# Kernel tuning notes

Measured on AMD Instinct MI355X. Metric: run time of the kernel, lower is better.

The kernel has to match this reference:

```python
import jax, jax.numpy as jnp
import numpy as np

N, E, T, R, L = 100000, 800000, 2, 4, 2
DIN, H, C, DOUT = 16, 256, 128, 4
EPS = 1e-5


def hetero_linear(x, node_type, W, b):
    # y[i] = x[i] @ W[node_type[i]] + b[node_type[i]]; small fixed T loop
    out = jnp.zeros((x.shape[0], W.shape[-1]), x.dtype)
    for t in range(W.shape[0]):
        out = out + jnp.where((node_type == t)[:, None], x @ W[t] + b[t], jnp.zeros((), x.dtype))
    return out


def hetero_bn(x, node_type, gamma, beta):
    # per-node-type batch norm (training-mode statistics, biased variance)
    T_ = gamma.shape[0]
    cnt = jax.ops.segment_sum(jnp.ones((x.shape[0],), x.dtype), node_type, num_segments=T_)
    cnt = jnp.maximum(cnt, 1.0)[:, None]
    mean = jax.ops.segment_sum(x, node_type, num_segments=T_) / cnt
    var = jax.ops.segment_sum(x * x, node_type, num_segments=T_) / cnt - mean * mean
    inv = jax.lax.rsqrt(var + EPS)
    return (x - mean[node_type]) * inv[node_type] * gamma[node_type] + beta[node_type]


def rgcn_conv(x, edge_index, edge_type, W, root, bias):
    # RGCNConv with sum aggregation: out_i = x_i @ root + b + sum_{(j->i), r} x_j @ W_r
    src, dst = edge_index[0], edge_index[1]
    hs = jnp.einsum('nd,rdf->rnf', x, W)          # [R, N, C]
    msg = hs[edge_type, src]                       # [E, C] per-edge relation-transformed source feats
    agg = jax.ops.segment_sum(msg, dst, num_segments=x.shape[0])
    return agg + x @ root + bias


def setup_inputs() -> dict:
    key = jax.random.key(0)
    ks = iter(jax.random.split(key, 40))

    def w(shape, fan_in):
        return jax.random.normal(next(ks), shape, jnp.float32) / np.float32(np.sqrt(fan_in))

    inp = {}
    inp['x'] = jax.random.normal(next(ks), (N, DIN), jnp.float32)
    inp['edge_index'] = jax.random.randint(next(ks), (2, E), 0, N)
    inp['node_type'] = jax.random.randint(next(ks), (N,), 0, T)
    inp['edge_type'] = jax.random.randint(next(ks), (E,), 0, R)
    inp['ri_w0'] = w((T, DIN, H), DIN); inp['ri_b0'] = jnp.zeros((T, H))
    inp['ri_g0'] = jnp.ones((T, H)); inp['ri_be0'] = jnp.zeros((T, H))
    inp['ri_w1'] = w((T, H, C), H); inp['ri_b1'] = jnp.zeros((T, C))
    inp['cn_g'] = jnp.ones((L, T, C)); inp['cn_b'] = jnp.zeros((L, T, C))
    inp['rg_w'] = w((L, R, C, C), C); inp['rg_root'] = w((L, C, C), C); inp['rg_bias'] = jnp.zeros((L, C))
    inp['mn_g'] = jnp.ones((L, T, C)); inp['mn_b'] = jnp.zeros((L, T, C))
    inp['mw0'] = w((L, T, C, H), C); inp['mb0'] = jnp.zeros((L, T, H))
    inp['mg0'] = jnp.ones((L, T, H)); inp['mbe0'] = jnp.zeros((L, T, H))
    inp['mw1'] = w((L, T, H, C), H); inp['mb1'] = jnp.zeros((L, T, C))
    inp['ro_w0'] = w((T, C, H), C); inp['ro_b0'] = jnp.zeros((T, H))
    inp['ro_g0'] = jnp.ones((T, H)); inp['ro_be0'] = jnp.zeros((T, H))
    inp['ro_w1'] = w((T, H, DOUT), H); inp['ro_b1'] = jnp.zeros((T, DOUT))
    return inp


def reference(x, edge_index, node_type, edge_type,
              ri_w0, ri_b0, ri_g0, ri_be0, ri_w1, ri_b1,
              cn_g, cn_b, rg_w, rg_root, rg_bias,
              mn_g, mn_b, mw0, mb0, mg0, mbe0, mw1, mb1,
              ro_w0, ro_b0, ro_g0, ro_be0, ro_w1, ro_b1):
    act = jax.nn.leaky_relu  # negative_slope 0.01, as nn.LeakyReLU default
    # readin MLP (plain_last)
    h = hetero_linear(x, node_type, ri_w0, ri_b0)
    h = act(hetero_bn(h, node_type, ri_g0, ri_be0))
    h = hetero_linear(h, node_type, ri_w1, ri_b1)
    # RES+ blocks: Norm -> Act -> Conv -> +res, Norm -> Act -> MLP -> +res (dropout=0)
    for l in range(rg_w.shape[0]):
        y = act(hetero_bn(h, node_type, cn_g[l], cn_b[l]))
        h = h + rgcn_conv(y, edge_index, edge_type, rg_w[l], rg_root[l], rg_bias[l])
        y = act(hetero_bn(h, node_type, mn_g[l], mn_b[l]))
        y = hetero_linear(y, node_type, mw0[l], mb0[l])
        y = act(hetero_bn(y, node_type, mg0[l], mbe0[l]))
        y = hetero_linear(y, node_type, mw1[l], mb1[l])
        h = h + y
    # readout MLP (plain_last)
    h = hetero_linear(h, node_type, ro_w0, ro_b0)
    h = act(hetero_bn(h, node_type, ro_g0, ro_be0))
    return hetero_linear(h, node_type, ro_w1, ro_b1)
```

## Files before the change

### kernel.cpp

```cpp
#include <hip/hip_runtime.h>

#define TT 2
#define RR 4
#define LL 2
#define DIN 16
#define HH 256
#define CC 128
#define DOUT 4
#define EPS 1e-5f
#define NB 32
#define NBG 16

typedef float v4f __attribute__((ext_vector_type(4)));
typedef short bf16x8 __attribute__((ext_vector_type(8)));

__device__ __forceinline__ ushort f2bf(float x) {
    uint u = __float_as_uint(x);
    return (ushort)((u + 0x7fffu + ((u >> 16) & 1u)) >> 16);
}
__device__ __forceinline__ float bf2f(ushort h) { return __uint_as_float(((uint)h) << 16); }
__device__ __forceinline__ int swc(int c) { return c ^ ((c >> 3) & 7); }
__device__ __forceinline__ uint pack2(float x, float y) {
    return (uint)f2bf(x) | ((uint)f2bf(y) << 16);
}

__global__ __launch_bounds__(1024) void k_scan1(const int* __restrict__ in, int* __restrict__ out,
                                                int* __restrict__ part, int n) {
    __shared__ int sm[1024];
    const int tid = threadIdx.x;
    const int i = blockIdx.x * 1024 + tid;
    const int v = (i < n) ? in[i] : 0;
    sm[tid] = v;
    __syncthreads();
    for (int off = 1; off < 1024; off <<= 1) {
        const int u = (tid >= off) ? sm[tid - off] : 0;
        __syncthreads();
        sm[tid] += u;
        __syncthreads();
    }
    if (i < n) out[i] = sm[tid] - v;
    if (tid == 1023) part[blockIdx.x] = sm[1023];
}

__global__ __launch_bounds__(1024) void k_scan2(int* __restrict__ part, int nb) {
    __shared__ int sm[1024];
    const int tid = threadIdx.x;
    const int v = (tid < nb) ? part[tid] : 0;
    sm[tid] = v;
    __syncthreads();
    for (int off = 1; off < 1024; off <<= 1) {
        const int u = (tid >= off) ? sm[tid - off] : 0;
        __syncthreads();
        sm[tid] += u;
        __syncthreads();
    }
    if (tid < nb) part[tid] = sm[tid] - v;
    if (tid == nb - 1) part[nb] = sm[tid];
}

__global__ __launch_bounds__(1024) void k_scan3(int* __restrict__ arr, const int* __restrict__ part,
                                                int n, int nb, int* __restrict__ typeStart,
                                                int* __restrict__ out2) {
    const int i = blockIdx.x * 1024 + threadIdx.x;
    if (i < n) {
        const int v = arr[i] + part[i >> 10];
        arr[i] = v;
        if (out2) out2[i] = v;
    } else if (i == n) {
        const int total = part[nb];
        arr[n] = total;
        if (typeStart) { typeStart[0] = 0; typeStart[1] = n - total; typeStart[2] = n; }
    }
}

__global__ __launch_bounds__(256) void k_build_perm(const int* __restrict__ nt, const int* __restrict__ pscan,
                                                    const int* __restrict__ typeStart, int* __restrict__ perm,
                                                    int* __restrict__ inv, int n) {
    const int i = blockIdx.x * 256 + threadIdx.x;
    if (i >= n) return;
    const int s1 = pscan[i];
    const int pos = nt[i] ? (typeStart[1] + s1) : (i - s1);
    perm[pos] = i;
    inv[i] = pos;
}

__global__ __launch_bounds__(256) void k_deg2(const int* __restrict__ dstv, const int* __restrict__ et,
                                              const int* __restrict__ inv, int* __restrict__ rowp2, int nE) {
    const int e = blockIdx.x * 256 + threadIdx.x;
    if (e < nE) atomicAdd(&rowp2[inv[dstv[e]] * 4 + et[e]], 1);
}

__global__ __launch_bounds__(256) void k_fill2(const int* __restrict__ srcv, const int* __restrict__ dstv,
                                               const int* __restrict__ et, const int* __restrict__ inv,
                                               int* __restrict__ cur, int* __restrict__ csr, int nE) {
    const int e = blockIdx.x * 256 + threadIdx.x;
    if (e < nE) {
        const int pos = atomicAdd(&cur[inv[dstv[e]] * 4 + et[e]], 1);
        csr[pos] = inv[srcv[e]];
    }
}

__global__ __launch_bounds__(256) void k_packall(const float* __restrict__ ri_w1, const float* __restrict__ mw0,
                                                 const float* __restrict__ mw1, const float* __restrict__ ro_w0,
                                                 ushort* __restrict__ p_ri1, ushort* __restrict__ p_mw0,
                                                 ushort* __restrict__ p_mw1, ushort* __restrict__ p_ro0) {
    for (long long idx = (long long)blockIdx.x * 256 + threadIdx.x; idx < 393216;
         idx += (long long)gridDim.x * 256) {
        const float* src; ushort* dst; int K, N; long long lo;
        if (idx < 65536)       { src = ri_w1; dst = p_ri1; K = 256; N = 128; lo = idx; }
        else if (idx < 196608) { src = mw0;   dst = p_mw0; K = 128; N = 256; lo = idx - 65536; }
        else if (idx < 327680) { src = mw1;   dst = p_mw1; K = 256; N = 128; lo = idx - 196608; }
        else                   { src = ro_w0; dst = p_ro0; K = 128; N = 256; lo = idx - 327680; }
        const int kn = K * N;
        const int mat = (int)(lo / kn);
        const int rem = (int)(lo - (long long)mat * kn);
        const int k = rem / N, col = rem % N;
        dst[((size_t)mat * (K / 8) + (k >> 3)) * N * 8 + (size_t)col * 8 + (k & 7)] = f2bf(src[lo]);
    }
}

__global__ __launch_bounds__(256) void k_pack_conv(const float* __restrict__ rgw_all,
                                                   const float* __restrict__ root_all,
                                                   ushort* __restrict__ dst_all) {
    const int idx = blockIdx.x * 256 + threadIdx.x;
    if (idx >= 640 * 128) return;
    const int l = blockIdx.y;
    const float* rgw = rgw_all + (size_t)l * RR * CC * CC;
    const float* root = root_all + (size_t)l * CC * CC;
    ushort* dst = dst_all + (size_t)l * 640 * 128;
    const int k = idx >> 7, col = idx & 127;
    const float v = (k < 512) ? rgw[(((k >> 7) * CC) + (k & 127)) * CC + col]
                              : root[(size_t)(k - 512) * CC + col];
    dst[((size_t)(k >> 3) * CC + col) * 8 + (k & 7)] = f2bf(v);
}

__global__ __launch_bounds__(512) void k_coef(const float* __restrict__ stat, const int* __restrict__ typeStart,
                                              const float* __restrict__ g, const float* __restrict__ be,
                                              float* __restrict__ scale, float* __restrict__ shift, int F) {
    const int tid = threadIdx.x;
    if (tid >= TT * F) return;
    const int t = tid / F;
    float s = 0.f, q = 0.f;
    for (int b = 0; b < NB; ++b) {
        s += stat[(size_t)b * 1024 + tid];
        q += stat[(size_t)b * 1024 + 512 + tid];
    }
    const float cnt = fmaxf((float)(typeStart[t + 1] - typeStart[t]), 1.f);
    const float mean = s / cnt;
    const float var = q / cnt - mean * mean;
    const float sc = g[tid] * rsqrtf(var + EPS);
    scale[tid] = sc;
    shift[tid] = be[tid] - mean * sc;
}

__global__ __launch_bounds__(256) void k_bnact(const float* __restrict__ h, const float* __restrict__ scale,
                                               const float* __restrict__ shift, const int* __restrict__ typeStart,
                                               ushort* __restrict__ y16, int n) {
    const int c0 = typeStart[1];
    const long long total = (long long)n * 32;
    for (long long idx = (long long)blockIdx.x * 256 + threadIdx.x; idx < total;
         idx += (long long)gridDim.x * 256) {
        const int i = (int)(idx >> 5), cq = (int)(idx & 31);
        const int t = (i >= c0) ? 1 : 0;
        const v4f v = *(const v4f*)(h + (size_t)i * CC + cq * 4);
        const v4f sc = *(const v4f*)(scale + t * CC + cq * 4);
        const v4f sf = *(const v4f*)(shift + t * CC + cq * 4);
        float o[4];
#pragma unroll
        for (int j = 0; j < 4; ++j) {
            const float vv = fmaf(v[j], sc[j], sf[j]);
            o[j] = fmaxf(vv, 0.01f * vv);
        }
        uint2 p = make_uint2(pack2(o[0], o[1]), pack2(o[2], o[3]));
        *(uint2*)((uint*)y16 + (size_t)i * 64 + cq * 2) = p;
    }
}

__global__ __launch_bounds__(256) void k_agg4(const ushort* __restrict__ y16, const int* __restrict__ rowp2,
                                              const int* __restrict__ csr, ushort* __restrict__ buf,
                                              int q0, int q1) {
    const int wid = threadIdx.x >> 6, lane = threadIdx.x & 63;
    const int i = q0 + blockIdx.x * 4 + wid;
    if (i >= q1) return;
    const uint* y32 = (const uint*)y16;
    float2 a0 = {0.f, 0.f}, a1 = {0.f, 0.f}, a2 = {0.f, 0.f}, a3 = {0.f, 0.f};
    const int e0 = rowp2[4 * i], b1 = rowp2[4 * i + 1], b2 = rowp2[4 * i + 2],
              b3 = rowp2[4 * i + 3], e1 = rowp2[4 * i + 4];
    for (int e = e0; e < e1; e += 64) {
        const int cnt = min(64, e1 - e);
        int pk = (lane < cnt) ? csr[e + lane] : 0;
        for (int j = 0; j < cnt; ++j) {
            const int s = __shfl(pk, j);
            const uint u = y32[(size_t)s * 64 + lane];
            const float vx = bf2f((ushort)(u & 0xffff));
            const float vy = bf2f((ushort)(u >> 16));
            const int idx = e + j;
            if (idx < b1)      { a0.x += vx; a0.y += vy; }
            else if (idx < b2) { a1.x += vx; a1.y += vy; }
            else if (idx < b3) { a2.x += vx; a2.y += vy; }
            else               { a3.x += vx; a3.y += vy; }
        }
    }
    uint* brow = (uint*)buf + (size_t)(i - q0) * 256;
    __builtin_nontemporal_store(pack2(a0.x, a0.y), brow + 0 * 64 + lane);
    __builtin_nontemporal_store(pack2(a1.x, a1.y), brow + 1 * 64 + lane);
    __builtin_nontemporal_store(pack2(a2.x, a2.y), brow + 2 * 64 + lane);
    __builtin_nontemporal_store(pack2(a3.x, a3.y), brow + 3 * 64 + lane);
}

__global__ __launch_bounds__(256) void k_gram(const float* __restrict__ x, const int* __restrict__ perm,
                                              const int* __restrict__ typeStart, float* __restrict__ gram) {
    __shared__ float Xs[256][17];
    const int tid = threadIdx.x;
    const int t = blockIdx.y;
    const int rbeg = typeStart[t], rend = typeStart[t + 1];
    const int r0 = rbeg + blockIdx.x * 1024;
    if (r0 >= rend) return;
    const int i = tid >> 4, j = tid & 15;
    float acc = 0.f, sacc = 0.f;
    for (int rr = 0; rr < 4; ++rr) {
        const int gr = r0 + rr * 256 + tid;
        v4f x0 = 0.f, x1 = 0.f, x2 = 0.f, x3 = 0.f;
        if (gr < rend) {
            const float* xr = x + (size_t)perm[gr] * DIN;
            x0 = *(const v4f*)xr; x1 = *(const v4f*)(xr + 4);
            x2 = *(const v4f*)(xr + 8); x3 = *(const v4f*)(xr + 12);
        }
        __syncthreads();
#pragma unroll
        for (int e = 0; e < 4; ++e) { Xs[tid][e] = x0[e]; Xs[tid][4 + e] = x1[e];
                                      Xs[tid][8 + e] = x2[e]; Xs[tid][12 + e] = x3[e]; }
        __syncthreads();
        for (int r = 0; r < 256; ++r) acc += Xs[r][i] * Xs[r][j];
        if (tid < 16)
            for (int r = 0; r < 256; ++r) sacc += Xs[r][tid];
        __syncthreads();
    }
    float* gb = gram + ((size_t)t * NBG + (blockIdx.x & (NBG - 1))) * 272;
    atomicAdd(&gb[tid], acc);
    if (tid < 16) atomicAdd(&gb[256 + tid], sacc);
}

__global__ __launch_bounds__(512) void k_ri_coef(const float* __restrict__ gram, const int* __restrict__ typeStart,
                                                 const float* __restrict__ ri_w0, const float* __restrict__ ri_b0,
                                                 const float* __restrict__ g, const float* __restrict__ be,
                                                 float* __restrict__ w0eff, float* __restrict__ b0eff) {
    __shared__ float G[2][272];
    const int tid = threadIdx.x;
    for (int idx = tid; idx < 2 * 272; idx += 512) {
        const int tt = idx / 272, k = idx % 272;
        float s = 0.f;
        for (int b = 0; b < NBG; ++b) s += gram[((size_t)tt * NBG + b) * 272 + k];
        G[tt][k] = s;
    }
    __syncthreads();
    const int t = tid >> 8, c = tid & 255;
    float wv[16];
#pragma unroll
    for (int k = 0; k < 16; ++k) wv[k] = ri_w0[((size_t)t * 16 + k) * HH + c];
    const float b = ri_b0[t * HH + c];
    const float cnt = fmaxf((float)(typeStart[t + 1] - typeStart[t]), 1.f);
    float sw = 0.f;
#pragma unroll
    for (int k = 0; k < 16; ++k) sw += G[t][256 + k] * wv[k];
    const float mean = (sw + cnt * b) / cnt;
    float e2 = 0.f;
#pragma unroll
    for (int i = 0; i < 16; ++i) {
        const float wi = wv[i];
#pragma unroll
        for (int j = 0; j < 16; ++j) e2 += wi * wv[j] * G[t][i * 16 + j];
    }
    e2 = (e2 + 2.f * b * sw + cnt * b * b) / cnt;
    const float var = e2 - mean * mean;
    const float sc = g[t * HH + c] * rsqrtf(var + EPS);
    const float sf = be[t * HH + c] - mean * sc;
    b0eff[t * HH + c] = b * sc + sf;
#pragma unroll
    for (int k = 0; k < 16; ++k) w0eff[((size_t)t * 16 + k) * HH + c] = wv[k] * sc;
}

__global__ __launch_bounds__(256) void k_readin(const float* __restrict__ x, const int* __restrict__ perm,
                                                const int* __restrict__ typeStart,
                                                const float* __restrict__ w0eff, const float* __restrict__ b0eff,
                                                const ushort* __restrict__ Wp, const float* __restrict__ b1,
                                                float* __restrict__ h, ushort* __restrict__ h16,
                                                float* __restrict__ stat) {
    __shared__ float Xs[128][17];
    __shared__ float W0s[16][256];
    __shared__ float b0s[256];
    __shared__ ushort As[128][40];
    __shared__ ushort Ws[4][128][8];

    const int tid = threadIdx.x;
    const int lane = tid & 63;
    const int wid = tid >> 6;
    const int woffm = (wid >> 1) * 64, woffn = (wid & 1) * 64;
    const int t = blockIdx.y;
    const int rbeg = typeStart[t], rend = typeStart[t + 1];
    const int r0 = rbeg + blockIdx.x * 128;
    if (r0 >= rend) return;

    for (int idx = tid; idx < 16 * 256; idx += 256) W0s[idx >> 8][idx & 255] = w0eff[(size_t)t * 4096 + idx];
    if (tid < 256) b0s[tid] = b0eff[t * 256 + tid];

    const int srow = tid >> 1, half = tid & 1;
    const int sgr = r0 + srow;
    const bool svalid = sgr < rend;
    {
        v4f x0 = 0.f, x1 = 0.f;
        if (svalid) {
            const float* xr = x + (size_t)perm[sgr] * DIN + half * 8;
            x0 = *(const v4f*)xr; x1 = *(const v4f*)(xr + 4);
        }
#pragma unroll
        for (int e = 0; e < 4; ++e) { Xs[srow][half * 8 + e] = x0[e]; Xs[srow][half * 8 + 4 + e] = x1[e]; }
    }
    __syncthreads();
    float xr[16];
#pragma unroll
    for (int k = 0; k < 16; ++k) xr[k] = Xs[srow][k];

    v4f acc[4][4];
#pragma unroll
    for (int mt = 0; mt < 4; ++mt)
#pragma unroll
        for (int nt = 0; nt < 4; ++nt) acc[mt][nt] = (v4f){0.f, 0.f, 0.f, 0.f};

    const size_t wmat = (size_t)t * 256 * 128;
    const int wcp = tid & 63;

    for (int kt = 0; kt < 8; ++kt) {
        const int k0 = kt * 32;
        ushort hA[16];
#pragma unroll
        for (int c2 = 0; c2 < 16; ++c2) {
            const int col = k0 + half * 16 + c2;
            float d = b0s[col];
#pragma unroll
            for (int k = 0; k < 16; ++k) d = fmaf(xr[k], W0s[k][col], d);
            d = fmaxf(d, 0.01f * d);
            hA[c2] = f2bf(d);
        }
        const ushort* wsrc = Wp + wmat + ((size_t)(k0 / 8 + wid) * 128) * 8 + (size_t)wcp * 16;
        const uint4 w0 = *(const uint4*)wsrc;
        const uint4 w1 = *(const uint4*)(wsrc + 8);
        __syncthreads();
        *(uint4*)&As[srow][half * 16] = *(uint4*)&hA[0];
        *(uint4*)&As[srow][half * 16 + 8] = *(uint4*)&hA[8];
        *(uint4*)&Ws[wid][swc(wcp * 2)][0] = w0;
        *(uint4*)&Ws[wid][swc(wcp * 2 + 1)][0] = w1;
        __syncthreads();
        const int afr = lane & 15;
        const int akg = (lane >> 4) * 8;
        bf16x8 aF[4], wf[4];
#pragma unroll
        for (int mt = 0; mt < 4; ++mt) aF[mt] = *(const bf16x8*)&As[woffm + mt * 16 + afr][akg];
#pragma unroll
        for (int nt = 0; nt < 4; ++nt) wf[nt] = *(const bf16x8*)&Ws[lane >> 4][swc(woffn + nt * 16 + afr)][0];
#pragma unroll
        for (int mt = 0; mt < 4; ++mt)
#pragma unroll
            for (int nt = 0; nt < 4; ++nt)
                acc[mt][nt] = __builtin_amdgcn_mfma_f32_16x16x32_bf16(aF[mt], wf[nt], acc[mt][nt], 0, 0, 0);
    }

    float bv[4];
#pragma unroll
    for (int nt = 0; nt < 4; ++nt) bv[nt] = b1[t * 128 + woffn + nt * 16 + (lane & 15)];
    float cs[4] = {0.f, 0.f, 0.f, 0.f}, cq[4] = {0.f, 0.f, 0.f, 0.f};
#pragma unroll
    for (int mt = 0; mt < 4; ++mt) {
        const int grow = r0 + woffm + mt * 16 + (lane >> 4) * 4;
#pragma unroll
        for (int nt = 0; nt < 4; ++nt) {
            const int gcol = woffn + nt * 16 + (lane & 15);
#pragma unroll
            for (int rg = 0; rg < 4; ++rg) {
                const int gr = grow + rg;
                if (gr < rend) {
                    const float v = acc[mt][nt][rg] + bv[nt];
                    const size_t o = (size_t)gr * 128 + gcol;
                    h[o] = v;
                    h16[o] = f2bf(v);
                    cs[nt] += v; cq[nt] += v * v;
                }
            }
        }
    }
    float* sb = stat + (size_t)(blockIdx.x & (NB - 1)) * 1024;
#pragma unroll
    for (int nt = 0; nt < 4; ++nt) {
        float s = cs[nt], q = cq[nt];
        s += __shfl_xor(s, 16); q += __shfl_xor(q, 16);
        s += __shfl_xor(s, 32); q += __shfl_xor(q, 32);
        if (lane < 16) {
            const int col = t * 128 + woffn + nt * 16 + lane;
            atomicAdd(&sb[col], s);
            atomicAdd(&sb[512 + col], q);
        }
    }
}

template <int K, int OUTW, bool TYPED, bool WHET, bool XBF, bool CROOT, bool BNIN,
          bool BHET, bool STATS, int OUTMODE>
__global__ __launch_bounds__(256) void k_mf(
    const float* __restrict__ Xf, const ushort* __restrict__ Xb, const ushort* __restrict__ Xb2,
    const ushort* __restrict__ Wp, const float* __restrict__ Bb,
    const float* __restrict__ scale, const float* __restrict__ shift,
    const int* __restrict__ typeStart, float* __restrict__ Y,
    ushort* __restrict__ Y16, float* __restrict__ stat,
    int rbase, int rbeg_u, int rend_u) {
    __shared__ ushort As[128][40];
    __shared__ ushort Ws[4][128][8];
    __shared__ float csh[BNIN ? K : 1];
    __shared__ float cfh[BNIN ? K : 1];

    constexpr int XSTR = CROOT ? 512 : K;

    const int tid = threadIdx.x;
    const int lane = tid & 63;
    const int wid = tid >> 6;
    const int woffm = (wid >> 1) * 64, woffn = (wid & 1) * 64;

    int t = 0, rbeg = rbeg_u, rend = rend_u;
    if constexpr (TYPED) { t = blockIdx.y; rbeg = typeStart[t]; rend = typeStart[t + 1]; }
    const int r0 = rbeg + blockIdx.x * 128;
    if (r0 >= rend) return;
    const int zoff = (OUTW == 256) ? blockIdx.z * 128 : 0;

    if constexpr (BNIN) {
        for (int k = tid; k < K; k += 256) { csh[k] = scale[t * K + k]; cfh[k] = shift[t * K + k]; }
        __syncthreads();
    }

    const int srow = tid >> 1, scg = (tid & 1) * 16;
    const int sgr = r0 + srow;
    const bool svalid = sgr < rend;
    const int wcp = tid & 63;

    v4f acc[4][4];
#pragma unroll
    for (int mt = 0; mt < 4; ++mt)
#pragma unroll
        for (int nt = 0; nt < 4; ++nt) acc[mt][nt] = (v4f){0.f, 0.f, 0.f, 0.f};

    const size_t wmat = (size_t)(WHET ? t : 0) * K * OUTW;

    for (int kt = 0; kt < K / 32; ++kt) {
        const int k0 = kt * 32;
        uint uu[8];
        if constexpr (XBF) {
            const ushort* xs;
            if constexpr (CROOT) {
                xs = (k0 >= 512) ? (Xb2 + (size_t)sgr * 128 + (k0 - 512) + scg)
                                 : (Xb + (size_t)(sgr - rbase) * XSTR + k0 + scg);
            } else {
                xs = Xb + (size_t)(sgr - rbase) * XSTR + k0 + scg;
            }
            uint4 a0 = make_uint4(0, 0, 0, 0), a1 = make_uint4(0, 0, 0, 0);
            if (svalid) {
                a0 = *(const uint4*)xs;
                a1 = *(const uint4*)(xs + 8);
            }
            uu[0] = a0.x; uu[1] = a0.y; uu[2] = a0.z; uu[3] = a0.w;
            uu[4] = a1.x; uu[5] = a1.y; uu[6] = a1.z; uu[7] = a1.w;
            if constexpr (BNIN) {
#pragma unroll
                for (int e = 0; e < 8; ++e) {
                    const int k = k0 + scg + 2 * e;
                    float f0 = fmaf(bf2f((ushort)(uu[e] & 0xffff)), csh[k], cfh[k]);
                    float f1 = fmaf(bf2f((ushort)(uu[e] >> 16)), csh[k + 1], cfh[k + 1]);
                    f0 = fmaxf(f0, 0.01f * f0);
                    f1 = fmaxf(f1, 0.01f * f1);
                    uu[e] = pack2(f0, f1);
                }
            }
        } else {
            float fv[16];
            {
                v4f av0 = 0.f, av1 = 0.f, av2 = 0.f, av3 = 0.f;
                if (svalid) {
                    const float* xs = Xf + (size_t)sgr * K + k0 + scg;
                    av0 = *(const v4f*)xs; av1 = *(const v4f*)(xs + 4);
                    av2 = *(const v4f*)(xs + 8); av3 = *(const v4f*)(xs + 12);
                }
#pragma unroll
                for (int e = 0; e < 4; ++e) { fv[e] = av0[e]; fv[4 + e] = av1[e];
                                              fv[8 + e] = av2[e]; fv[12 + e] = av3[e]; }
            }
            if constexpr (BNIN) {
#pragma unroll
                for (int e = 0; e < 16; ++e) {
                    const int k = k0 + scg + e;
                    float vv = fmaf(fv[e], csh[k], cfh[k]);
                    fv[e] = fmaxf(vv, 0.01f * vv);
                }
            }
#pragma unroll
            for (int e = 0; e < 8; ++e) uu[e] = pack2(fv[2 * e], fv[2 * e + 1]);
        }
        const ushort* wsrc = Wp + wmat + ((size_t)(k0 / 8 + wid) * OUTW + zoff) * 8 + (size_t)wcp * 16;
        const uint4 w0 = *(const uint4*)wsrc;
        const uint4 w1 = *(const uint4*)(wsrc + 8);

        __syncthreads();
        *(uint4*)&As[srow][scg] = make_uint4(uu[0], uu[1], uu[2], uu[3]);
        *(uint4*)&As[srow][scg + 8] = make_uint4(uu[4], uu[5], uu[6], uu[7]);
        *(uint4*)&Ws[wid][swc(wcp * 2)][0] = w0;
        *(uint4*)&Ws[wid][swc(wcp * 2 + 1)][0] = w1;
        __syncthreads();

        const int afr = lane & 15;
        const int akg = (lane >> 4) * 8;
        bf16x8 aF[4], wf[4];
#pragma unroll
        for (int mt = 0; mt < 4; ++mt) aF[mt] = *(const bf16x8*)&As[woffm + mt * 16 + afr][akg];
#pragma unroll
        for (int nt = 0; nt < 4; ++nt) wf[nt] = *(const bf16x8*)&Ws[lane >> 4][swc(woffn + nt * 16 + afr)][0];
#pragma unroll
        for (int mt = 0; mt < 4; ++mt)
#pragma unroll
            for (int nt = 0; nt < 4; ++nt)
                acc[mt][nt] = __builtin_amdgcn_mfma_f32_16x16x32_bf16(aF[mt], wf[nt], acc[mt][nt], 0, 0, 0);
    }

    const float* BbT = Bb + (BHET ? (size_t)t * OUTW : 0);
    float bv[4];
#pragma unroll
    for (int nt = 0; nt < 4; ++nt) bv[nt] = BbT[zoff + woffn + nt * 16 + (lane & 15)];
    const int c0 = (STATS && !TYPED) ? typeStart[1] : 0;
    float cs0[4] = {0.f, 0.f, 0.f, 0.f}, cq0[4] = {0.f, 0.f, 0.f, 0.f};
    float cs1[4] = {0.f, 0.f, 0.f, 0.f}, cq1[4] = {0.f, 0.f, 0.f, 0.f};
#pragma unroll
    for (int mt = 0; mt < 4; ++mt) {
        const int grow = r0 + woffm + mt * 16 + (lane >> 4) * 4;
#pragma unroll
        for (int nt = 0; nt < 4; ++nt) {
            const int gcol = zoff + woffn + nt * 16 + (lane & 15);
#pragma unroll
            for (int rg = 0; rg < 4; ++rg) {
                const int gr = grow + rg;
                if (gr < rend) {
                    float v = acc[mt][nt][rg] + bv[nt];
                    const size_t o = (size_t)gr * OUTW + gcol;
                    if constexpr (OUTMODE == 0) Y[o] = v;
                    if constexpr (OUTMODE == 1) Y16[o] = f2bf(v);
                    if constexpr (OUTMODE == 2) {
                        const float hv = Y[o] + v;
                        Y[o] = hv;
                        Y16[o] = f2bf(hv);
                        v = hv;
                    }
                    if constexpr (STATS) {
                        if (TYPED || gr < c0) { cs0[nt] += v; cq0[nt] += v * v; }
                        else                  { cs1[nt] += v; cq1[nt] += v * v; }
                    }
                }
            }
        }
    }
    if constexpr (STATS) {
        float* sb = stat + (size_t)(blockIdx.x & (NB - 1)) * 1024;
#pragma unroll
        for (int nt = 0; nt < 4; ++nt) {
            float s = cs0[nt], q = cq0[nt];
            s += __shfl_xor(s, 16); q += __shfl_xor(q, 16);
            s += __shfl_xor(s, 32); q += __shfl_xor(q, 32);
            if (lane < 16) {
                const int col = t * OUTW + zoff + woffn + nt * 16 + lane;
                atomicAdd(&sb[col], s);
                atomicAdd(&sb[512 + col], q);
            }
            if constexpr (!TYPED) {
                float s1 = cs1[nt], q1 = cq1[nt];
                s1 += __shfl_xor(s1, 16); q1 += __shfl_xor(q1, 16);
                s1 += __shfl_xor(s1, 32); q1 += __shfl_xor(q1, 32);
                if (lane < 16) {
                    const int col = OUTW + zoff + woffn + nt * 16 + lane;
                    atomicAdd(&sb[col], s1);
                    atomicAdd(&sb[512 + col], q1);
                }
            }
        }
    }
}

__global__ __launch_bounds__(256) void k_ro1(const ushort* __restrict__ A256b, const int* __restrict__ perm,
                                             const int* __restrict__ typeStart, const float* __restrict__ ro_w1,
                                             const float* __restrict__ ro_b1, const float* __restrict__ scale,
                                             const float* __restrict__ shift, float* __restrict__ out, int n) {
    __shared__ float W1s[2][256][4];
    __shared__ float scs[512];
    __shared__ float sfs[512];
    const int tid = threadIdx.x;
    for (int idx = tid; idx < 2048; idx += 256) {
        const int t = idx >> 10, rem = idx & 1023;
        W1s[t][rem >> 2][rem & 3] = ro_w1[idx];
    }
    for (int idx = tid; idx < 512; idx += 256) { scs[idx] = scale[idx]; sfs[idx] = shift[idx]; }
    __syncthreads();
    const int trow = tid >> 2, sub = tid & 3;
    const int gr = blockIdx.x * 64 + trow;
    if (gr >= n) return;
    const int c0 = typeStart[1];
    const int t = (gr >= c0) ? 1 : 0;
    v4f acc = 0.f;
    const ushort* ar = A256b + (size_t)gr * 256 + sub * 64;
#pragma unroll
    for (int q = 0; q < 8; ++q) {
        const uint4 u = *(const uint4*)(ar + q * 8);
        const uint uw[4] = {u.x, u.y, u.z, u.w};
#pragma unroll
        for (int e = 0; e < 4; ++e) {
#pragma unroll
            for (int hl = 0; hl < 2; ++hl) {
                const int col = sub * 64 + q * 8 + 2 * e + hl;
                const float v = bf2f((ushort)(hl ? (uw[e] >> 16) : (uw[e] & 0xffff)));
                float vv = fmaf(v, scs[t * 256 + col], sfs[t * 256 + col]);
                vv = fmaxf(vv, 0.01f * vv);
                acc += vv * *(const v4f*)&W1s[t][col][0];
            }
        }
    }
#pragma unroll
    for (int e = 0; e < 4; ++e) { acc[e] += __shfl_xor(acc[e], 1); acc[e] += __shfl_xor(acc[e], 2); }
    if (sub == 0) {
        acc += *(const v4f*)(ro_b1 + t * 4);
        *(v4f*)(out + (size_t)perm[gr] * 4) = acc;
    }
}

extern "C" void kernel_launch(void* const* d_in, const int* in_sizes, int n_in,
                              void* d_out, int out_size, void* d_ws, size_t ws_size,
                              hipStream_t stream) {
    const float* x = (const float*)d_in[0];
    const int* ei = (const int*)d_in[1];
    const int* nt = (const int*)d_in[2];
    const int* et = (const int*)d_in[3];
    const float* ri_w0 = (const float*)d_in[4];
    const float* ri_b0 = (const float*)d_in[5];
    const float* ri_g0 = (const float*)d_in[6];
    const float* ri_be0 = (const float*)d_in[7];
    const float* ri_w1 = (const float*)d_in[8];
    const float* ri_b1 = (const float*)d_in[9];
    const float* cn_g = (const float*)d_in[10];
    const float* cn_b = (const float*)d_in[11];
    const float* rg_w = (const float*)d_in[12];
    const float* rg_root = (const float*)d_in[13];
    const float* rg_bias = (const float*)d_in[14];
    const float* mn_g = (const float*)d_in[15];
    const float* mn_b = (const float*)d_in[16];
    const float* mw0 = (const float*)d_in[17];
    const float* mb0 = (const float*)d_in[18];
    const float* mg0 = (const float*)d_in[19];
    const float* mbe0 = (const float*)d_in[20];
    const float* mw1 = (const float*)d_in[21];
    const float* mb1 = (const float*)d_in[22];
    const float* ro_w0 = (const float*)d_in[23];
    const float* ro_b0 = (const float*)d_in[24];
    const float* ro_g0 = (const float*)d_in[25];
    const float* ro_be0 = (const float*)d_in[26];
    const float* ro_w1 = (const float*)d_in[27];
    const float* ro_b1 = (const float*)d_in[28];

    const int n = in_sizes[2];
    const int nE = in_sizes[3];
    const int* srcv = ei;
    const int* dstv = ei + nE;

    char* w = (char*)d_ws;
    size_t off = 0;
    auto alloc = [&](size_t bytes) -> char* {
        char* p = w + off;
        off = (off + bytes + 255) & ~(size_t)255;
        return p;
    };
    float* h = (float*)alloc((size_t)n * CC * sizeof(float));
    ushort* h16 = (ushort*)alloc((size_t)n * CC * sizeof(ushort));
    int* csr = (int*)alloc((size_t)nE * sizeof(int));
    int* rowp2 = (int*)alloc(((size_t)4 * n + 1) * sizeof(int));
    int* cur2 = (int*)alloc((size_t)4 * n * sizeof(int));
    int* perm = (int*)alloc((size_t)n * sizeof(int));
    int* inv = (int*)alloc((size_t)n * sizeof(int));
    int* pscan = (int*)alloc((size_t)(n + 1) * sizeof(int));
    int* part = (int*)alloc(2052 * sizeof(int));
    int* typeStart = (int*)alloc(64);
    float* statgram = (float*)alloc(((size_t)9 * NB * 1024 + 2 * NBG * 272) * sizeof(float));
    float* scale = (float*)alloc(512 * sizeof(float));
    float* shift = (float*)alloc(512 * sizeof(float));
    float* w0eff = (float*)alloc((size_t)2 * 16 * 256 * sizeof(float));
    float* b0eff = (float*)alloc(512 * sizeof(float));
    ushort* pw_ri1 = (ushort*)alloc(65536 * 2);
    ushort* pw_mw0 = (ushort*)alloc(131072 * 2);
    ushort* pw_mw1 = (ushort*)alloc(131072 * 2);
    ushort* pw_ro0 = (ushort*)alloc(65536 * 2);
    ushort* pw_conv = (ushort*)alloc(163840 * 2);
    char* region2 = alloc((size_t)n * 512);
    if (ws_size < off) return;

    float* statbuf = statgram;
    float* gram = statgram + (size_t)9 * NB * 1024;
    ushort* A256b = (ushort*)region2;
    ushort* y16 = (ushort*)region2;
    float* out = (float*)d_out;

    ushort* buf = (ushort*)(w + off);
    const size_t bufBytes = (ws_size > off) ? (ws_size - off) : 0;
    const long long chkcap = (long long)(bufBytes / 1024);
    if (chkcap < 1024) return;
    int nchunk, CHK;
    if (chkcap >= n) { nchunk = 1; CHK = n; }
    else { nchunk = (int)((n + chkcap - 1) / chkcap); CHK = (n + nchunk - 1) / nchunk; }

    auto SS = [&](int slot) { return statbuf + (size_t)slot * NB * 1024; };

    const int gE = (nE + 255) / 256;
    const int gN = (n + 255) / 256;
    const int nb = (n + 1023) / 1024;
    const int m4 = 4 * n;
    const int nb2 = (m4 + 1023) / 1024;
    const int gmx = (n + 127) / 128;

    k_packall<<<1536, 256, 0, stream>>>(ri_w1, mw0, mw1, ro_w0, pw_ri1, pw_mw0, pw_mw1, pw_ro0);
    k_pack_conv<<<dim3(320, 2), 256, 0, stream>>>(rg_w, rg_root, pw_conv);

    hipMemsetAsync(statgram, 0, ((size_t)9 * NB * 1024 + 2 * NBG * 272) * sizeof(float), stream);
    k_scan1<<<nb, 1024, 0, stream>>>(nt, pscan, part, n);
    k_scan2<<<1, 1024, 0, stream>>>(part, nb);
    k_scan3<<<(n + 1024) / 1024, 1024, 0, stream>>>(pscan, part, n, nb, typeStart, nullptr);
    k_build_perm<<<gN, 256, 0, stream>>>(nt, pscan, typeStart, perm, inv, n);
    hipMemsetAsync(rowp2, 0, ((size_t)m4 + 1) * sizeof(int), stream);
    k_deg2<<<gE, 256, 0, stream>>>(dstv, et, inv, rowp2, nE);
    k_scan1<<<nb2, 1024, 0, stream>>>(rowp2, rowp2, part, m4);
    k_scan2<<<1, 1024, 0, stream>>>(part, nb2);
    k_scan3<<<(m4 + 1024) / 1024, 1024, 0, stream>>>(rowp2, part, m4, nb2, nullptr, cur2);
    k_fill2<<<gE, 256, 0, stream>>>(srcv, dstv, et, inv, cur2, csr, nE);

    k_gram<<<dim3((n + 1023) / 1024, 2), 256, 0, stream>>>(x, perm, typeStart, gram);
    k_ri_coef<<<1, 512, 0, stream>>>(gram, typeStart, ri_w0, ri_b0, ri_g0, ri_be0, w0eff, b0eff);
    k_readin<<<dim3(gmx, 2), 256, 0, stream>>>(x, perm, typeStart, w0eff, b0eff, pw_ri1, ri_b1,
                                               h, h16, SS(1));

    for (int l = 0; l < LL; ++l) {
        const int s_cn = l ? 4 : 1, s_mn = l ? 5 : 2, s_mg = l ? 6 : 3, s_nx = l ? 7 : 4;
        k_coef<<<1, 512, 0, stream>>>(SS(s_cn), typeStart, cn_g + (size_t)l * TT * CC,
                                      cn_b + (size_t)l * TT * CC, scale, shift, CC);
        k_bnact<<<4096, 256, 0, stream>>>(h, scale, shift, typeStart, y16, n);
        const ushort* wconv = pw_conv + (size_t)l * 640 * 128;
        for (int q0 = 0; q0 < n; q0 += CHK) {
            const int q1 = min(n, q0 + CHK);
            k_agg4<<<(q1 - q0 + 3) / 4, 256, 0, stream>>>(y16, rowp2, csr, buf, q0, q1);
            k_mf<640, 128, false, false, true, true, false, false, true, 2>
                <<<(q1 - q0 + 127) / 128, 256, 0, stream>>>(
                    nullptr, buf, y16, wconv, rg_bias + (size_t)l * CC, nullptr, nullptr,
                    typeStart, h, h16, SS(s_mn), q0, q0, q1);
        }

        k_coef<<<1, 512, 0, stream>>>(SS(s_mn), typeStart, mn_g + (size_t)l * TT * CC,
                                      mn_b + (size_t)l * TT * CC, scale, shift, CC);
        k_mf<128, 256, true, true, true, false, true, true, true, 1><<<dim3(gmx, 2, 2), 256, 0, stream>>>(
            nullptr, h16, nullptr, pw_mw0 + (size_t)l * 2 * 128 * 256, mb0 + (size_t)l * TT * HH,
            scale, shift, typeStart, nullptr, A256b, SS(s_mg), 0, 0, n);
        k_coef<<<1, 512, 0, stream>>>(SS(s_mg), typeStart, mg0 + (size_t)l * TT * HH,
                                      mbe0 + (size_t)l * TT * HH, scale, shift, HH);
        if (l == 0)
            k_mf<256, 128, true, true, true, false, true, true, true, 2><<<dim3(gmx, 2, 1), 256, 0, stream>>>(
                nullptr, A256b, nullptr, pw_mw1 + (size_t)l * 2 * 256 * 128, mb1 + (size_t)l * TT * CC,
                scale, shift, typeStart, h, h16, SS(s_nx), 0, 0, n);
        else
            k_mf<256, 128, true, true, true, false, true, true, false, 2><<<dim3(gmx, 2, 1), 256, 0, stream>>>(
                nullptr, A256b, nullptr, pw_mw1 + (size_t)l * 2 * 256 * 128, mb1 + (size_t)l * TT * CC,
                scale, shift, typeStart, h, h16, nullptr, 0, 0, n);
    }

    k_mf<128, 256, true, true, true, false, false, true, true, 1><<<dim3(gmx, 2, 2), 256, 0, stream>>>(
        nullptr, h16, nullptr, pw_ro0, ro_b0, nullptr, nullptr, typeStart, nullptr, A256b, SS(8), 0, 0, n);
    k_coef<<<1, 512, 0, stream>>>(SS(8), typeStart, ro_g0, ro_be0, scale, shift, HH);
    k_ro1<<<(n + 63) / 64, 256, 0, stream>>>(A256b, perm, typeStart, ro_w1, ro_b1, scale, shift, out, n);
}
```

Baseline: 801.6 us.

## Load MFMA operands directly from global memory, dropping LDS staging in k_mf

Restructures the bf16 MFMA GEMM kernel so each wave owns 32 rows by 128 columns and loads A fragments and packed weight fragments straight from global memory into registers. This removes the shared-memory tiles and the two __syncthreads per k-step. The float-input path is dropped, the k loop is fully unrolled, and buffers gain 128 padding rows so unguarded loads stay in bounds. In exchange, weight fragments are no longer shared through LDS, so each wave reads the full weight tile from global or L2 memory, and register pressure rises.

```diff
diff --git a/kernel.cpp b/kernel.cpp
--- a/kernel.cpp
+++ b/kernel.cpp
@@ -402,17 +402,15 @@
     }
 }
 
-template <int K, int OUTW, bool TYPED, bool WHET, bool XBF, bool CROOT, bool BNIN,
+template <int K, int OUTW, bool TYPED, bool WHET, bool CROOT, bool BNIN,
           bool BHET, bool STATS, int OUTMODE>
 __global__ __launch_bounds__(256) void k_mf(
-    const float* __restrict__ Xf, const ushort* __restrict__ Xb, const ushort* __restrict__ Xb2,
+    const ushort* __restrict__ Xb, const ushort* __restrict__ Xb2,
     const ushort* __restrict__ Wp, const float* __restrict__ Bb,
     const float* __restrict__ scale, const float* __restrict__ shift,
     const int* __restrict__ typeStart, float* __restrict__ Y,
     ushort* __restrict__ Y16, float* __restrict__ stat,
     int rbase, int rbeg_u, int rend_u) {
-    __shared__ ushort As[128][40];
-    __shared__ ushort Ws[4][128][8];
     __shared__ float csh[BNIN ? K : 1];
     __shared__ float cfh[BNIN ? K : 1];
 
@@ -421,7 +419,8 @@
     const int tid = threadIdx.x;
     const int lane = tid & 63;
     const int wid = tid >> 6;
-    const int woffm = (wid >> 1) * 64, woffn = (wid & 1) * 64;
+    const int kgrp = lane >> 4;
+    const int fr = lane & 15;
 
     int t = 0, rbeg = rbeg_u, rend = rend_u;
     if constexpr (TYPED) { t = blockIdx.y; rbeg = typeStart[t]; rend = typeStart[t + 1]; }
@@ -434,110 +433,77 @@
         __syncthreads();
     }
 
-    const int srow = tid >> 1, scg = (tid & 1) * 16;
-    const int sgr = r0 + srow;
-    const bool svalid = sgr < rend;
-    const int wcp = tid & 63;
-
-    v4f acc[4][4];
-#pragma unroll
-    for (int mt = 0; mt < 4; ++mt)
-#pragma unroll
-        for (int nt = 0; nt < 4; ++nt) acc[mt][nt] = (v4f){0.f, 0.f, 0.f, 0.f};
+    const int row0 = r0 + wid * 32 + fr;
+    const int row1 = row0 + 16;
+    const bool v0 = row0 < rend, v1 = row1 < rend;
+
+    v4f acc[2][8];
+#pragma unroll
+    for (int mt = 0; mt < 2; ++mt)
+#pragma unroll
+        for (int nt = 0; nt < 8; ++nt) acc[mt][nt] = (v4f){0.f, 0.f, 0.f, 0.f};
 
     const size_t wmat = (size_t)(WHET ? t : 0) * K * OUTW;
 
+#pragma unroll
     for (int kt = 0; kt < K / 32; ++kt) {
         const int k0 = kt * 32;
-        uint uu[8];
-        if constexpr (XBF) {
-            const ushort* xs;
-            if constexpr (CROOT) {
-                xs = (k0 >= 512) ? (Xb2 + (size_t)sgr * 128 + (k0 - 512) + scg)
-                                 : (Xb + (size_t)(sgr - rbase) * XSTR + k0 + scg);
+        const int kk = k0 + kgrp * 8;
+        uint4 a0 = make_uint4(0, 0, 0, 0), a1 = make_uint4(0, 0, 0, 0);
+        if constexpr (CROOT) {
+            if (k0 >= 512) {
+                const int co = (k0 - 512) + kgrp * 8;
+                if (v0) a0 = *(const uint4*)(Xb2 + (size_t)row0 * 128 + co);
+                if (v1) a1 = *(const uint4*)(Xb2 + (size_t)row1 * 128 + co);
             } else {
-                xs = Xb + (size_t)(sgr - rbase) * XSTR + k0 + scg;
-            }
-            uint4 a0 = make_uint4(0, 0, 0, 0), a1 = make_uint4(0, 0, 0, 0);
-            if (svalid) {
-                a0 = *(const uint4*)xs;
-                a1 = *(const uint4*)(xs + 8);
-            }
-            uu[0] = a0.x; uu[1] = a0.y; uu[2] = a0.z; uu[3] = a0.w;
-            uu[4] = a1.x; uu[5] = a1.y; uu[6] = a1.z; uu[7] = a1.w;
-            if constexpr (BNIN) {
-#pragma unroll
-                for (int e = 0; e < 8; ++e) {
-                    const int k = k0 + scg + 2 * e;
-                    float f0 = fmaf(bf2f((ushort)(uu[e] & 0xffff)), csh[k], cfh[k]);
-                    float f1 = fmaf(bf2f((ushort)(uu[e] >> 16)), csh[k + 1], cfh[k + 1]);
-                    f0 = fmaxf(f0, 0.01f * f0);
-                    f1 = fmaxf(f1, 0.01f * f1);
-                    uu[e] = pack2(f0, f1);
-                }
+                if (v0) a0 = *(const uint4*)(Xb + (size_t)(row0 - rbase) * XSTR + kk);
+                if (v1) a1 = *(const uint4*)(Xb + (size_t)(row1 - rbase) * XSTR + kk);
             }
         } else {
-            float fv[16];
-            {
-                v4f av0 = 0.f, av1 = 0.f, av2 = 0.f, av3 = 0.f;
-                if (svalid) {
-                    const float* xs = Xf + (size_t)sgr * K + k0 + scg;
-                    av0 = *(const v4f*)xs; av1 = *(const v4f*)(xs + 4);
-                    av2 = *(const v4f*)(xs + 8); av3 = *(const v4f*)(xs + 12);
-                }
-#pragma unroll
-                for (int e = 0; e < 4; ++e) { fv[e] = av0[e]; fv[4 + e] = av1[e];
-                                              fv[8 + e] = av2[e]; fv[12 + e] = av3[e]; }
+            if (v0) a0 = *(const uint4*)(Xb + (size_t)(row0 - rbase) * XSTR + kk);
+            if (v1) a1 = *(const uint4*)(Xb + (size_t)(row1 - rbase) * XSTR + kk);
+        }
+        if constexpr (BNIN) {
+            uint ua[8] = {a0.x, a0.y, a0.z, a0.w, a1.x, a1.y, a1.z, a1.w};
+#pragma unroll
+            for (int e = 0; e < 8; ++e) {
+                const int k = kk + 2 * (e & 3);
+                float f0 = fmaf(bf2f((ushort)(ua[e] & 0xffff)), csh[k], cfh[k]);
+                float f1 = fmaf(bf2f((ushort)(ua[e] >> 16)), csh[k + 1], cfh[k + 1]);
+                f0 = fmaxf(f0, 0.01f * f0);
+                f1 = fmaxf(f1, 0.01f * f1);
+                ua[e] = pack2(f0, f1);
             }
-            if constexpr (BNIN) {
-#pragma unroll
-                for (int e = 0; e < 16; ++e) {
-                    const int k = k0 + scg + e;
-                    float vv = fmaf(fv[e], csh[k], cfh[k]);
-                    fv[e] = fmaxf(vv, 0.01f * vv);
-                }
-            }
-#pragma unroll
-            for (int e = 0; e < 8; ++e) uu[e] = pack2(fv[2 * e], fv[2 * e + 1]);
-        }
-        const ushort* wsrc = Wp + wmat + ((size_t)(k0 / 8 + wid) * OUTW + zoff) * 8 + (size_t)wcp * 16;
-        const uint4 w0 = *(const uint4*)wsrc;
-        const uint4 w1 = *(const uint4*)(wsrc + 8);
-
-        __syncthreads();
-        *(uint4*)&As[srow][scg] = make_uint4(uu[0], uu[1], uu[2], uu[3]);
-        *(uint4*)&As[srow][scg + 8] = make_uint4(uu[4], uu[5], uu[6], uu[7]);
-        *(uint4*)&Ws[wid][swc(wcp * 2)][0] = w0;
-        *(uint4*)&Ws[wid][swc(wcp * 2 + 1)][0] = w1;
-        __syncthreads();
-
-        const int afr = lane & 15;
-        const int akg = (lane >> 4) * 8;
-        bf16x8 aF[4], wf[4];
-#pragma unroll
-        for (int mt = 0; mt < 4; ++mt) aF[mt] = *(const bf16x8*)&As[woffm + mt * 16 + afr][akg];
-#pragma unroll
-        for (int nt = 0; nt < 4; ++nt) wf[nt] = *(const bf16x8*)&Ws[lane >> 4][swc(woffn + nt * 16 + afr)][0];
-#pragma unroll
-        for (int mt = 0; mt < 4; ++mt)
-#pragma unroll
-            for (int nt = 0; nt < 4; ++nt)
-                acc[mt][nt] = __builtin_amdgcn_mfma_f32_16x16x32_bf16(aF[mt], wf[nt], acc[mt][nt], 0, 0, 0);
+            a0 = make_uint4(ua[0], ua[1], ua[2], ua[3]);
+            a1 = make_uint4(ua[4], ua[5], ua[6], ua[7]);
+        }
+        const bf16x8 aF0 = *(const bf16x8*)&a0;
+        const bf16x8 aF1 = *(const bf16x8*)&a1;
+        const ushort* wk = Wp + wmat + ((size_t)(k0 / 8 + kgrp) * OUTW + zoff + fr) * 8;
+        bf16x8 wf[8];
+#pragma unroll
+        for (int nt = 0; nt < 8; ++nt) wf[nt] = *(const bf16x8*)(wk + (size_t)nt * 128);
+#pragma unroll
+        for (int nt = 0; nt < 8; ++nt) {
+            acc[0][nt] = __builtin_amdgcn_mfma_f32_16x16x32_bf16(aF0, wf[nt], acc[0][nt], 0, 0, 0);
+            acc[1][nt] = __builtin_amdgcn_mfma_f32_16x16x32_bf16(aF1, wf[nt], acc[1][nt], 0, 0, 0);
+        }
     }
 
     const float* BbT = Bb + (BHET ? (size_t)t * OUTW : 0);
-    float bv[4];
-#pragma unroll
-    for (int nt = 0; nt < 4; ++nt) bv[nt] = BbT[zoff + woffn + nt * 16 + (lane & 15)];
+    float bv[8];
+#pragma unroll
+    for (int nt = 0; nt < 8; ++nt) bv[nt] = BbT[zoff + nt * 16 + fr];
     const int c0 = (STATS && !TYPED) ? typeStart[1] : 0;
-    float cs0[4] = {0.f, 0.f, 0.f, 0.f}, cq0[4] = {0.f, 0.f, 0.f, 0.f};
-    float cs1[4] = {0.f, 0.f, 0.f, 0.f}, cq1[4] = {0.f, 0.f, 0.f, 0.f};
-#pragma unroll
-    for (int mt = 0; mt < 4; ++mt) {
-        const int grow = r0 + woffm + mt * 16 + (lane >> 4) * 4;
-#pragma unroll
-        for (int nt = 0; nt < 4; ++nt) {
-            const int gcol = zoff + woffn + nt * 16 + (lane & 15);
+    float cs0[8], cq0[8], cs1[8], cq1[8];
+#pragma unroll
+    for (int nt = 0; nt < 8; ++nt) { cs0[nt] = 0.f; cq0[nt] = 0.f; cs1[nt] = 0.f; cq1[nt] = 0.f; }
+#pragma unroll
+    for (int mt = 0; mt < 2; ++mt) {
+        const int grow = r0 + wid * 32 + mt * 16 + kgrp * 4;
+#pragma unroll
+        for (int nt = 0; nt < 8; ++nt) {
+            const int gcol = zoff + nt * 16 + fr;
 #pragma unroll
             for (int rg = 0; rg < 4; ++rg) {
                 const int gr = grow + rg;
@@ -563,12 +529,12 @@
     if constexpr (STATS) {
         float* sb = stat + (size_t)(blockIdx.x & (NB - 1)) * 1024;
 #pragma unroll
-        for (int nt = 0; nt < 4; ++nt) {
+        for (int nt = 0; nt < 8; ++nt) {
             float s = cs0[nt], q = cq0[nt];
             s += __shfl_xor(s, 16); q += __shfl_xor(q, 16);
             s += __shfl_xor(s, 32); q += __shfl_xor(q, 32);
             if (lane < 16) {
-                const int col = t * OUTW + zoff + woffn + nt * 16 + lane;
+                const int col = t * OUTW + zoff + nt * 16 + lane;
                 atomicAdd(&sb[col], s);
                 atomicAdd(&sb[512 + col], q);
             }
@@ -577,7 +543,7 @@
                 s1 += __shfl_xor(s1, 16); q1 += __shfl_xor(q1, 16);
                 s1 += __shfl_xor(s1, 32); q1 += __shfl_xor(q1, 32);
                 if (lane < 16) {
-                    const int col = OUTW + zoff + woffn + nt * 16 + lane;
+                    const int col = OUTW + zoff + nt * 16 + lane;
                     atomicAdd(&sb[col], s1);
                     atomicAdd(&sb[512 + col], q1);
                 }
@@ -677,7 +643,7 @@
         return p;
     };
     float* h = (float*)alloc((size_t)n * CC * sizeof(float));
-    ushort* h16 = (ushort*)alloc((size_t)n * CC * sizeof(ushort));
+    ushort* h16 = (ushort*)alloc((size_t)(n + 128) * CC * sizeof(ushort));
     int* csr = (int*)alloc((size_t)nE * sizeof(int));
     int* rowp2 = (int*)alloc(((size_t)4 * n + 1) * sizeof(int));
     int* cur2 = (int*)alloc((size_t)4 * n * sizeof(int));
@@ -696,7 +662,7 @@
     ushort* pw_mw1 = (ushort*)alloc(131072 * 2);
     ushort* pw_ro0 = (ushort*)alloc(65536 * 2);
     ushort* pw_conv = (ushort*)alloc(163840 * 2);
-    char* region2 = alloc((size_t)n * 512);
+    char* region2 = alloc((size_t)(n + 128) * 512);
     if (ws_size < off) return;
 
     float* statbuf = statgram;
@@ -707,7 +673,7 @@
 
     ushort* buf = (ushort*)(w + off);
     const size_t bufBytes = (ws_size > off) ? (ws_size - off) : 0;
-    const long long chkcap = (long long)(bufBytes / 1024);
+    const long long chkcap = (long long)(bufBytes / 1024) - 128;
     if (chkcap < 1024) return;
     int nchunk, CHK;
     if (chkcap >= n) { nchunk = 1; CHK = n; }
@@ -751,31 +717,31 @@
         for (int q0 = 0; q0 < n; q0 += CHK) {
             const int q1 = min(n, q0 + CHK);
             k_agg4<<<(q1 - q0 + 3) / 4, 256, 0, stream>>>(y16, rowp2, csr, buf, q0, q1);
-            k_mf<640, 128, false, false, true, true, false, false, true, 2>
+            k_mf<640, 128, false, false, true, false, false, true, 2>
                 <<<(q1 - q0 + 127) / 128, 256, 0, stream>>>(
-                    nullptr, buf, y16, wconv, rg_bias + (size_t)l * CC, nullptr, nullptr,
+                    buf, y16, wconv, rg_bias + (size_t)l * CC, nullptr, nullptr,
                     typeStart, h, h16, SS(s_mn), q0, q0, q1);
         }
 
         k_coef<<<1, 512, 0, stream>>>(SS(s_mn), typeStart, mn_g + (size_t)l * TT * CC,
                                       mn_b + (size_t)l * TT * CC, scale, shift, CC);
-        k_mf<128, 256, true, true, true, false, true, true, true, 1><<<dim3(gmx, 2, 2), 256, 0, stream>>>(
-            nullptr, h16, nullptr, pw_mw0 + (size_t)l * 2 * 128 * 256, mb0 + (size_t)l * TT * HH,
+        k_mf<128, 256, true, true, false, true, true, true, 1><<<dim3(gmx, 2, 2), 256, 0, stream>>>(
+            h16, nullptr, pw_mw0 + (size_t)l * 2 * 128 * 256, mb0 + (size_t)l * TT * HH,
             scale, shift, typeStart, nullptr, A256b, SS(s_mg), 0, 0, n);
         k_coef<<<1, 512, 0, stream>>>(SS(s_mg), typeStart, mg0 + (size_t)l * TT * HH,
                                       mbe0 + (size_t)l * TT * HH, scale, shift, HH);
         if (l == 0)
-            k_mf<256, 128, true, true, true, false, true, true, true, 2><<<dim3(gmx, 2, 1), 256, 0, stream>>>(
-                nullptr, A256b, nullptr, pw_mw1 + (size_t)l * 2 * 256 * 128, mb1 + (size_t)l * TT * CC,
+            k_mf<256, 128, true, true, false, true, true, true, 2><<<dim3(gmx, 2, 1), 256, 0, stream>>>(
+                A256b, nullptr, pw_mw1 + (size_t)l * 2 * 256 * 128, mb1 + (size_t)l * TT * CC,
                 scale, shift, typeStart, h, h16, SS(s_nx), 0, 0, n);
         else
-            k_mf<256, 128, true, true, true, false, true, true, false, 2><<<dim3(gmx, 2, 1), 256, 0, stream>>>(
-                nullptr, A256b, nullptr, pw_mw1 + (size_t)l * 2 * 256 * 128, mb1 + (size_t)l * TT * CC,
+            k_mf<256, 128, true, true, false, true, true, false, 2><<<dim3(gmx, 2, 1), 256, 0, stream>>>(
+                A256b, nullptr, pw_mw1 + (size_t)l * 2 * 256 * 128, mb1 + (size_t)l * TT * CC,
                 scale, shift, typeStart, h, h16, nullptr, 0, 0, n);
     }
 
-    k_mf<128, 256, true, true, true, false, false, true, true, 1><<<dim3(gmx, 2, 2), 256, 0, stream>>>(
-        nullptr, h16, nullptr, pw_ro0, ro_b0, nullptr, nullptr, typeStart, nullptr, A256b, SS(8), 0, 0, n);
+    k_mf<128, 256, true, true, false, false, true, true, 1><<<dim3(gmx, 2, 2), 256, 0, stream>>>(
+        h16, nullptr, pw_ro0, ro_b0, nullptr, nullptr, typeStart, nullptr, A256b, SS(8), 0, 0, n);
     k_coef<<<1, 512, 0, stream>>>(SS(8), typeStart, ro_g0, ro_be0, scale, shift, HH);
     k_ro1<<<(n + 63) / 64, 256, 0, stream>>>(A256b, perm, typeStart, ro_w1, ro_b1, scale, shift, out, n);
 }
```

Result: slower. 907.3 us (+13.2%).
